# Kernel tuning notes

Hardware: AMD Instinct MI355X
Metric: run time of the kernel (lower is better)

Reference implementation:

```python
import jax, jax.numpy as jnp
import numpy as np

N = 100000          # nodes
E = 3200000         # edges per order (avg degree 32)
F_IN = 512          # num_features
HID = 128           # args.hidden
ORDER = 2
K = 10              # propagation hops
ALPHA = 0.1
C = 10              # num_classes


def setup_inputs() -> dict:
    key = jax.random.key(0)
    ks = jax.random.split(key, 10)
    x = jax.random.normal(ks[0], (N, F_IN), dtype=jnp.float32)
    edge_index1 = jax.random.randint(ks[1], (2, E), 0, N, dtype=jnp.int32)
    edge_weight1 = jax.random.uniform(ks[2], (E,), dtype=jnp.float32) / 32.0  # ~row-normalized
    edge_index2 = jax.random.randint(ks[3], (2, E), 0, N, dtype=jnp.int32)
    edge_weight2 = jax.random.uniform(ks[4], (E,), dtype=jnp.float32) / 32.0
    W_in = jax.random.normal(ks[5], (ORDER, F_IN, HID), dtype=jnp.float32) * 0.05
    b_in = jnp.zeros((ORDER, HID), dtype=jnp.float32)
    # GPR filter weights: fW[k] = alpha*(1-alpha)^k, fW[K] = (1-alpha)^K
    k_arr = np.arange(K + 1, dtype=np.float32)
    fw = ALPHA * (1.0 - ALPHA) ** k_arr
    fw[-1] = (1.0 - ALPHA) ** K
    fW = jnp.broadcast_to(jnp.asarray(fw), (ORDER, K + 1)).astype(jnp.float32)
    W_out = jax.random.normal(ks[6], (HID * ORDER, C), dtype=jnp.float32) * 0.05
    b_out = jnp.zeros((C,), dtype=jnp.float32)
    return {"x": x, "edge_index1": edge_index1, "edge_weight1": edge_weight1,
            "edge_index2": edge_index2, "edge_weight2": edge_weight2,
            "W_in": W_in, "b_in": b_in, "fW": fW, "W_out": W_out, "b_out": b_out}


def _spmm(edge_index, edge_weight, h, n):
    # y[row] += w * h[col]  (COO SpMM with add-aggregation)
    row, col = edge_index[0], edge_index[1]
    return jax.ops.segment_sum(edge_weight[:, None] * h[col], row, num_segments=n)


def reference(x, edge_index1, edge_weight1, edge_index2, edge_weight2,
              W_in, b_in, fW, W_out, b_out):
    n = x.shape[0]
    branches = [(edge_index1, edge_weight1), (edge_index2, edge_weight2)]
    outs = []
    for i, (ei, ew) in enumerate(branches):
        h = x @ W_in[i] + b_in[i]                 # [N, HID]  (dropout inactive in eval)
        hidden = h * fW[i, 0]
        for k in range(K):                        # K-hop GPR-weighted propagation
            h = _spmm(ei, ew, h, n)
            hidden = hidden + fW[i, k + 1] * h
        outs.append(hidden)
    z = jnp.concatenate(outs, axis=1) @ W_out + b_out   # [N, C]
    return jax.nn.log_softmax(z, axis=1)
```

## Files before the change

### kernel.cpp

```cpp
#include <hip/hip_runtime.h>

#define F_IN 512
#define HID 128
#define KHOPS 10
#define COUT 10
#define BM 64
#define BK 16
#define COLMASK 0x1FFFF

typedef unsigned int uint;

__device__ __forceinline__ uint f2bf1(float f) {
    uint u = __float_as_uint(f);
    return (u + 0x7fffu + ((u >> 16) & 1u)) >> 16;
}
__device__ __forceinline__ uint packbf(float a, float b) {
    return f2bf1(a) | (f2bf1(b) << 16);
}
__device__ __forceinline__ float bflo(uint u) { return __uint_as_float(u << 16); }
__device__ __forceinline__ float bfhi(uint u) { return __uint_as_float(u & 0xffff0000u); }

__global__ __launch_bounds__(256) void gemm_in_kernel(
    const float* __restrict__ x, const float* __restrict__ Win,
    const float* __restrict__ bin, uint* __restrict__ h1, uint* __restrict__ h2, int n)
{
    const int br = blockIdx.y;
    const float* W = Win + (size_t)br * F_IN * HID;
    const float* bias = bin + (size_t)br * HID;
    uint* h = br ? h2 : h1;

    __shared__ float xs[BM][BK + 1];
    __shared__ float wsb[BK][HID];
    const int t = threadIdx.x;
    const int row0 = blockIdx.x * BM;
    const int ty = t >> 4, tx = t & 15;

    float acc[4][8];
#pragma unroll
    for (int i = 0; i < 4; ++i)
#pragma unroll
        for (int j = 0; j < 8; ++j) acc[i][j] = 0.f;

    const int xr = t >> 2;
    const int xk = (t & 3) * 4;

    for (int k0 = 0; k0 < F_IN; k0 += BK) {
        float4 xv = make_float4(0.f, 0.f, 0.f, 0.f);
        if (row0 + xr < n)
            xv = *(const float4*)(x + (size_t)(row0 + xr) * F_IN + k0 + xk);
        xs[xr][xk] = xv.x; xs[xr][xk + 1] = xv.y;
        xs[xr][xk + 2] = xv.z; xs[xr][xk + 3] = xv.w;
#pragma unroll
        for (int rep = 0; rep < 2; ++rep) {
            int idx = t + rep * 256;
            int kr = idx >> 5;
            int c4 = (idx & 31) * 4;
            *(float4*)(&wsb[kr][c4]) = *(const float4*)(W + (size_t)(k0 + kr) * HID + c4);
        }
        __syncthreads();
#pragma unroll
        for (int kk = 0; kk < BK; ++kk) {
            float a0 = xs[ty * 4 + 0][kk];
            float a1 = xs[ty * 4 + 1][kk];
            float a2 = xs[ty * 4 + 2][kk];
            float a3 = xs[ty * 4 + 3][kk];
            const float4 b0 = *(const float4*)(&wsb[kk][tx * 8]);
            const float4 b1 = *(const float4*)(&wsb[kk][tx * 8 + 4]);
            acc[0][0] = fmaf(a0, b0.x, acc[0][0]); acc[0][1] = fmaf(a0, b0.y, acc[0][1]);
            acc[0][2] = fmaf(a0, b0.z, acc[0][2]); acc[0][3] = fmaf(a0, b0.w, acc[0][3]);
            acc[0][4] = fmaf(a0, b1.x, acc[0][4]); acc[0][5] = fmaf(a0, b1.y, acc[0][5]);
            acc[0][6] = fmaf(a0, b1.z, acc[0][6]); acc[0][7] = fmaf(a0, b1.w, acc[0][7]);
            acc[1][0] = fmaf(a1, b0.x, acc[1][0]); acc[1][1] = fmaf(a1, b0.y, acc[1][1]);
            acc[1][2] = fmaf(a1, b0.z, acc[1][2]); acc[1][3] = fmaf(a1, b0.w, acc[1][3]);
            acc[1][4] = fmaf(a1, b1.x, acc[1][4]); acc[1][5] = fmaf(a1, b1.y, acc[1][5]);
            acc[1][6] = fmaf(a1, b1.z, acc[1][6]); acc[1][7] = fmaf(a1, b1.w, acc[1][7]);
            acc[2][0] = fmaf(a2, b0.x, acc[2][0]); acc[2][1] = fmaf(a2, b0.y, acc[2][1]);
            acc[2][2] = fmaf(a2, b0.z, acc[2][2]); acc[2][3] = fmaf(a2, b0.w, acc[2][3]);
            acc[2][4] = fmaf(a2, b1.x, acc[2][4]); acc[2][5] = fmaf(a2, b1.y, acc[2][5]);
            acc[2][6] = fmaf(a2, b1.z, acc[2][6]); acc[2][7] = fmaf(a2, b1.w, acc[2][7]);
            acc[3][0] = fmaf(a3, b0.x, acc[3][0]); acc[3][1] = fmaf(a3, b0.y, acc[3][1]);
            acc[3][2] = fmaf(a3, b0.z, acc[3][2]); acc[3][3] = fmaf(a3, b0.w, acc[3][3]);
            acc[3][4] = fmaf(a3, b1.x, acc[3][4]); acc[3][5] = fmaf(a3, b1.y, acc[3][5]);
            acc[3][6] = fmaf(a3, b1.z, acc[3][6]); acc[3][7] = fmaf(a3, b1.w, acc[3][7]);
        }
        __syncthreads();
    }

    const float4 bv0 = *(const float4*)(bias + tx * 8);
    const float4 bv1 = *(const float4*)(bias + tx * 8 + 4);
#pragma unroll
    for (int i = 0; i < 4; ++i) {
        int row = row0 + ty * 4 + i;
        if (row >= n) continue;
        uint4 o;
        o.x = packbf(acc[i][0] + bv0.x, acc[i][1] + bv0.y);
        o.y = packbf(acc[i][2] + bv0.z, acc[i][3] + bv0.w);
        o.z = packbf(acc[i][4] + bv1.x, acc[i][5] + bv1.y);
        o.w = packbf(acc[i][6] + bv1.z, acc[i][7] + bv1.w);
        *(uint4*)(h + (size_t)row * 64 + tx * 4) = o;
    }
}


__global__ void bhist_kernel(const int* __restrict__ r1, int E1,
                             const int* __restrict__ r2, int E2,
                             int* __restrict__ bcnt, int nb)
{
    extern __shared__ int sh[];
    const int br = blockIdx.y;
    const int* rows = br ? r2 : r1;
    const int E = br ? E2 : E1;
    int* bc = bcnt + (size_t)br * nb;
    for (int i = threadIdx.x; i < nb; i += blockDim.x) sh[i] = 0;
    __syncthreads();
    for (int i = blockIdx.x * blockDim.x + threadIdx.x; i < E; i += gridDim.x * blockDim.x)
        atomicAdd(&sh[rows[i] >> 6], 1);
    __syncthreads();
    for (int i = threadIdx.x; i < nb; i += blockDim.x)
        if (sh[i]) atomicAdd(&bc[i], sh[i]);
}

__global__ __launch_bounds__(256) void bscan_kernel(
    const int* __restrict__ bcnt, int* __restrict__ bbase, int* __restrict__ bcur,
    int* __restrict__ rowp1, int* __restrict__ rowp2,
    int nb, int n, int E1, int E2)
{
    __shared__ int ssum[256];
    const int br = blockIdx.y;
    const int* bc = bcnt + (size_t)br * nb;
    int* bb = bbase + (size_t)br * (nb + 1);
    int* cur = bcur + (size_t)br * nb;
    int* rowp = br ? rowp2 : rowp1;
    const int E = br ? E2 : E1;
    const int t = threadIdx.x;
    const int chunk = (nb + 255) / 256;
    const int start = t * chunk;
    const int end = (start + chunk < nb) ? start + chunk : nb;
    int sum = 0;
    for (int i = start; i < end; ++i) sum += bc[i];
    ssum[t] = sum;
    __syncthreads();
    if (t == 0) {
        int run = 0;
        for (int i = 0; i < 256; ++i) { int v = ssum[i]; ssum[i] = run; run += v; }
        bb[nb] = E;
        rowp[n] = E;
    }
    __syncthreads();
    int run = ssum[t];
    for (int i = start; i < end; ++i) {
        bb[i] = run; cur[i] = run; run += bc[i];
    }
}

#define SCAT_BLOCKS 256
__global__ __launch_bounds__(256) void bscat_kernel(
    const int* __restrict__ r1, const int* __restrict__ c1, const float* __restrict__ w1, int E1,
    const int* __restrict__ r2, const int* __restrict__ c2, const float* __restrict__ w2, int E2,
    int* __restrict__ bcur, int2* __restrict__ t1, int2* __restrict__ t2, int nb)
{
    extern __shared__ int sh[];
    int* lh = sh;
    int* lbase = sh + nb;
    const int br = blockIdx.y;
    const int* rows = br ? r2 : r1;
    const int* cols = br ? c2 : c1;
    const float* w  = br ? w2 : w1;
    const int E = br ? E2 : E1;
    int* cur = bcur + (size_t)br * nb;
    int2* tcw = br ? t2 : t1;
    const int t = threadIdx.x;

    for (int i = t; i < nb; i += 256) lh[i] = 0;
    __syncthreads();

    const int per = (E + SCAT_BLOCKS - 1) / SCAT_BLOCKS;
    const int c0 = blockIdx.x * per;
    const int cend = (c0 + per < E) ? c0 + per : E;

    for (int i = c0 + t; i < cend; i += 256)
        atomicAdd(&lh[rows[i] >> 6], 1);
    __syncthreads();
    for (int b = t; b < nb; b += 256) {
        int c = lh[b];
        lbase[b] = c ? atomicAdd(&cur[b], c) : 0;
        lh[b] = 0;
    }
    __syncthreads();
    for (int i = c0 + t; i < cend; i += 256) {
        int r = rows[i];
        int b = r >> 6;
        int p = atomicAdd(&lh[b], 1);
        uint lo = (uint)cols[i] | ((uint)(r & 63) << 17);
        tcw[lbase[b] + p] = make_int2((int)lo, __float_as_int(w[i]));
    }
}

__global__ __launch_bounds__(256) void bsort_kernel(
    const int* __restrict__ bbase,
    const int2* __restrict__ t1, const int2* __restrict__ t2,
    int* __restrict__ rowp1, int* __restrict__ rowp2,
    int2* __restrict__ cw1, int2* __restrict__ cw2, int nb, int n)
{
    __shared__ int cnt[64], soff[64], pos[64];
    const int br = blockIdx.y;
    const int* bb = bbase + (size_t)br * (nb + 1);
    const int2* tcw = br ? t2 : t1;
    int* rowp = br ? rowp2 : rowp1;
    int2* cw = br ? cw2 : cw1;
    const int b = blockIdx.x;
    const int t = threadIdx.x;
    const int base = bb[b];
    const int m = bb[b + 1] - base;
    if (t < 64) cnt[t] = 0;
    __syncthreads();
    for (int i = t; i < m; i += 256) atomicAdd(&cnt[((uint)tcw[base + i].x >> 17) & 63], 1);
    __syncthreads();
    if (t == 0) {
        int run = 0;
#pragma unroll
        for (int r = 0; r < 64; ++r) { soff[r] = run; run += cnt[r]; }
    }
    __syncthreads();
    if (t < 64) {
        pos[t] = soff[t];
        int g = b * 64 + t;
        if (g < n) rowp[g] = base + soff[t];
    }
    __syncthreads();
    for (int i = t; i < m; i += 256) {
        int2 e = tcw[base + i];
        int r = ((uint)e.x >> 17) & 63;
        int p = atomicAdd(&pos[r], 1);
        cw[base + p] = e;
    }
}

struct BrArgs {
    const int* rowp;
    const int2* cw;
    const uint* hin;
    uint* hout;
    const float* Wo;
};

__global__ __launch_bounds__(256) void spmm2_kernel(
    BrArgs A, BrArgs B, const float* __restrict__ fW, int k,
    float* __restrict__ z2, int storeH, int n)
{
    const int bid = blockIdx.x;
    const int br = bid & 1;
    const int wid = (bid >> 1) * 4 + (threadIdx.x >> 6);
    if (wid >= n) return;
    const int*   rowp = br ? B.rowp : A.rowp;
    const int2*  cw   = br ? B.cw   : A.cw;
    const uint*  hin  = br ? B.hin  : A.hin;
    uint*        hout = br ? B.hout : A.hout;
    const float* Wo   = br ? B.Wo   : A.Wo;
    const int lane = threadIdx.x & 63;

    float w0[COUT], w1[COUT];
    const float* wp = Wo + (size_t)(lane * 2) * COUT;
#pragma unroll
    for (int c = 0; c < COUT; ++c) { w0[c] = wp[c]; w1[c] = wp[COUT + c]; }

    const int s = rowp[wid];
    const int e = rowp[wid + 1];
    const uint* hb = hin + lane;

    float2 acc = make_float2(0.f, 0.f);
    int i = s;
    while (i < e) {
        const int rem = e - i;
        const int cnt = rem < 64 ? rem : 64;
        int2 my = make_int2(0, 0);
        if (lane < cnt) my = cw[i + lane];
        int j = 0;
        for (; j + 3 < cnt; j += 4) {
            const int x0 = __builtin_amdgcn_readlane(my.x, j);
            const int y0 = __builtin_amdgcn_readlane(my.y, j);
            const int x1 = __builtin_amdgcn_readlane(my.x, j + 1);
            const int y1 = __builtin_amdgcn_readlane(my.y, j + 1);
            const int x2 = __builtin_amdgcn_readlane(my.x, j + 2);
            const int y2 = __builtin_amdgcn_readlane(my.y, j + 2);
            const int x3 = __builtin_amdgcn_readlane(my.x, j + 3);
            const int y3 = __builtin_amdgcn_readlane(my.y, j + 3);
            const uint g0 = hb[(size_t)(x0 & COLMASK) * 64];
            const uint g1 = hb[(size_t)(x1 & COLMASK) * 64];
            const uint g2 = hb[(size_t)(x2 & COLMASK) * 64];
            const uint g3 = hb[(size_t)(x3 & COLMASK) * 64];
            const float q0 = __int_as_float(y0), q1 = __int_as_float(y1);
            const float q2 = __int_as_float(y2), q3 = __int_as_float(y3);
            acc.x = fmaf(q0, bflo(g0), acc.x); acc.y = fmaf(q0, bfhi(g0), acc.y);
            acc.x = fmaf(q1, bflo(g1), acc.x); acc.y = fmaf(q1, bfhi(g1), acc.y);
            acc.x = fmaf(q2, bflo(g2), acc.x); acc.y = fmaf(q2, bfhi(g2), acc.y);
            acc.x = fmaf(q3, bflo(g3), acc.x); acc.y = fmaf(q3, bfhi(g3), acc.y);
        }
        for (; j < cnt; ++j) {
            const int xj = __builtin_amdgcn_readlane(my.x, j);
            const int yj = __builtin_amdgcn_readlane(my.y, j);
            const uint g = hb[(size_t)(xj & COLMASK) * 64];
            const float q = __int_as_float(yj);
            acc.x = fmaf(q, bflo(g), acc.x);
            acc.y = fmaf(q, bfhi(g), acc.y);
        }
        i += cnt;
    }

    if (storeH)
        hout[(size_t)wid * 64 + lane] = packbf(acc.x, acc.y);

    const float fw = fW[br * (KHOPS + 1) + k + 1];
    float zadd = 0.f;
#pragma unroll
    for (int c = 0; c < COUT; ++c) {
        float pp = fmaf(acc.x, w0[c], acc.y * w1[c]);
#pragma unroll
        for (int off = 32; off; off >>= 1) pp += __shfl_xor(pp, off);
        if (lane == c) zadd = pp;
    }
    if (lane < COUT) {
        const size_t o = (size_t)wid * (2 * COUT) + br * COUT + lane;
        z2[o] += fw * zadd;
    }
}

__global__ __launch_bounds__(256) void zacc2_kernel(
    const uint* __restrict__ h1, const uint* __restrict__ h2,
    const float* __restrict__ Wout, const float* __restrict__ fW,
    float* __restrict__ z2, int n)
{
    const int wid = (blockIdx.x * blockDim.x + threadIdx.x) >> 6;
    if (wid >= n) return;
    const int lane = threadIdx.x & 63;
    const uint u1 = h1[(size_t)wid * 64 + lane];
    const uint u2 = h2[(size_t)wid * 64 + lane];
    const float a1 = bflo(u1), b1v = bfhi(u1);
    const float a2 = bflo(u2), b2v = bfhi(u2);
    const float* wp1 = Wout + (size_t)(lane * 2) * COUT;
    const float* wp2 = Wout + (size_t)HID * COUT + (size_t)(lane * 2) * COUT;
    float zv1 = 0.f, zv2 = 0.f;
#pragma unroll
    for (int c = 0; c < COUT; ++c) {
        float p1 = fmaf(a1, wp1[c], b1v * wp1[COUT + c]);
        float p2 = fmaf(a2, wp2[c], b2v * wp2[COUT + c]);
#pragma unroll
        for (int off = 32; off; off >>= 1) { p1 += __shfl_xor(p1, off); p2 += __shfl_xor(p2, off); }
        if (lane == c) { zv1 = p1; zv2 = p2; }
    }
    if (lane < COUT) {
        z2[(size_t)wid * (2 * COUT) + lane]        = fW[0] * zv1;
        z2[(size_t)wid * (2 * COUT) + COUT + lane] = fW[KHOPS + 1] * zv2;
    }
}

__global__ void logsm_kernel(const float* __restrict__ z2, const float* __restrict__ bout,
                             float* __restrict__ out, int n)
{
    const int r = blockIdx.x * blockDim.x + threadIdx.x;
    if (r >= n) return;
    float v[COUT];
    float m = -1e30f;
#pragma unroll
    for (int c = 0; c < COUT; ++c) {
        v[c] = z2[(size_t)r * (2 * COUT) + c] + z2[(size_t)r * (2 * COUT) + COUT + c] + bout[c];
        m = fmaxf(m, v[c]);
    }
    float s = 0.f;
#pragma unroll
    for (int c = 0; c < COUT; ++c) s += expf(v[c] - m);
    const float l = logf(s) + m;
#pragma unroll
    for (int c = 0; c < COUT; ++c) out[(size_t)r * COUT + c] = v[c] - l;
}

extern "C" void kernel_launch(void* const* d_in, const int* in_sizes, int n_in,
                              void* d_out, int out_size, void* d_ws, size_t ws_size,
                              hipStream_t stream)
{
    const float* x    = (const float*)d_in[0];
    const int*   ei1  = (const int*)d_in[1];
    const float* ew1  = (const float*)d_in[2];
    const int*   ei2  = (const int*)d_in[3];
    const float* ew2  = (const float*)d_in[4];
    const float* Win  = (const float*)d_in[5];
    const float* bin  = (const float*)d_in[6];
    const float* fW   = (const float*)d_in[7];
    const float* Wout = (const float*)d_in[8];
    const float* bout = (const float*)d_in[9];
    const int n  = in_sizes[0] / F_IN;
    const int E1 = in_sizes[2];
    const int E2 = in_sizes[4];
    const int Emax = E1 > E2 ? E1 : E2;
    const int nb = (n + 63) / 64;
    float* zout = (float*)d_out;

    char* p = (char*)d_ws;
    auto alloc = [&](size_t bytes) { char* r = p; p += (bytes + 255) & ~(size_t)255; return r; };
    char* regA = alloc((size_t)4 * n * 64 * 4);
    uint* h1A = (uint*)regA;
    uint* h1B = (uint*)(regA + (size_t)n * 64 * 4);
    uint* h2A = (uint*)(regA + (size_t)2 * n * 64 * 4);
    uint* h2B = (uint*)(regA + (size_t)3 * n * 64 * 4);
    int2* tcw1 = (int2*)regA;
    int2* tcw2 = (int2*)(regA + (size_t)Emax * 8);
    int2* cw1  = (int2*)alloc((size_t)Emax * 8);
    int2* cw2  = (int2*)alloc((size_t)Emax * 8);
    int*  rowp1 = (int*)alloc((size_t)(n + 1) * 4);
    int*  rowp2 = (int*)alloc((size_t)(n + 1) * 4);
    float* z2  = (float*)alloc((size_t)n * 2 * COUT * 4);
    int*  bcnt  = (int*)alloc((size_t)2 * nb * 4);
    int*  bbase = (int*)alloc((size_t)2 * (nb + 1) * 4);
    int*  bcur  = (int*)alloc((size_t)2 * nb * 4);

    const int rowBlocks = (n + 3) / 4;

    hipMemsetAsync(bcnt, 0, (size_t)2 * nb * 4, stream);
    hipLaunchKernelGGL(bhist_kernel, dim3(256, 2), dim3(256), nb * 4, stream,
                       ei1, E1, ei2, E2, bcnt, nb);
    hipLaunchKernelGGL(bscan_kernel, dim3(1, 2), dim3(256), 0, stream,
                       bcnt, bbase, bcur, rowp1, rowp2, nb, n, E1, E2);
    hipLaunchKernelGGL(bscat_kernel, dim3(SCAT_BLOCKS, 2), dim3(256), 2 * nb * 4, stream,
                       ei1, ei1 + E1, ew1, E1, ei2, ei2 + E2, ew2, E2,
                       bcur, tcw1, tcw2, nb);
    hipLaunchKernelGGL(bsort_kernel, dim3(nb, 2), dim3(256), 0, stream,
                       bbase, tcw1, tcw2, rowp1, rowp2, cw1, cw2, nb, n);

    hipLaunchKernelGGL(gemm_in_kernel, dim3((n + BM - 1) / BM, 2), dim3(256), 0, stream,
                       x, Win, bin, h1A, h2A, n);

    hipLaunchKernelGGL(zacc2_kernel, dim3(rowBlocks), dim3(256), 0, stream,
                       h1A, h2A, Wout, fW, z2, n);

    uint* cur1 = h1A; uint* nxt1 = h1B;
    uint* cur2 = h2A; uint* nxt2 = h2B;
    for (int k = 0; k < KHOPS; ++k) {
        const int storeH = (k < KHOPS - 1) ? 1 : 0;
        BrArgs A { rowp1, cw1, cur1, nxt1, Wout };
        BrArgs B { rowp2, cw2, cur2, nxt2, Wout + (size_t)HID * COUT };
        hipLaunchKernelGGL(spmm2_kernel, dim3(rowBlocks * 2), dim3(256), 0, stream,
                           A, B, fW, k, z2, storeH, n);
        uint* t1 = cur1; cur1 = nxt1; nxt1 = t1;
        uint* t2 = cur2; cur2 = nxt2; nxt2 = t2;
    }

    hipLaunchKernelGGL(logsm_kernel, dim3((n + 255) / 256), dim3(256), 0, stream,
                       z2, bout, zout, n);
}
```

Before: 2.959 ms.

## Replace FP32 input GEMM with bf16 MFMA kernel using pre-swizzled weights

After: 2.662 ms. 10.0% less time.

```diff
diff --git a/kernel.cpp b/kernel.cpp
--- a/kernel.cpp
+++ b/kernel.cpp
@@ -4,11 +4,12 @@
 #define HID 128
 #define KHOPS 10
 #define COUT 10
-#define BM 64
-#define BK 16
 #define COLMASK 0x1FFFF
 
 typedef unsigned int uint;
+typedef unsigned short ushort;
+typedef float f32x4 __attribute__((ext_vector_type(4)));
+typedef short bf16x8 __attribute__((ext_vector_type(8)));
 
 __device__ __forceinline__ uint f2bf1(float f) {
     uint u = __float_as_uint(f);
@@ -20,87 +21,89 @@
 __device__ __forceinline__ float bflo(uint u) { return __uint_as_float(u << 16); }
 __device__ __forceinline__ float bfhi(uint u) { return __uint_as_float(u & 0xffff0000u); }
 
-__global__ __launch_bounds__(256) void gemm_in_kernel(
-    const float* __restrict__ x, const float* __restrict__ Win,
+__global__ __launch_bounds__(256) void wprep_kernel(
+    const float* __restrict__ Win, ushort* __restrict__ Wsw)
+{
+    const int t = blockIdx.x * blockDim.x + threadIdx.x;
+    if (t >= 2 * 16 * 8 * 64) return;
+    const int l = t & 63;
+    const int c = (t >> 6) & 7;
+    const int s = (t >> 9) & 15;
+    const int br = t >> 13;
+    const int col = c * 16 + (l & 15);
+    const int k0 = s * 32 + (l >> 4) * 8;
+    const float* W = Win + (size_t)br * F_IN * HID;
+    uint o0 = packbf(W[(size_t)(k0 + 0) * HID + col], W[(size_t)(k0 + 1) * HID + col]);
+    uint o1 = packbf(W[(size_t)(k0 + 2) * HID + col], W[(size_t)(k0 + 3) * HID + col]);
+    uint o2 = packbf(W[(size_t)(k0 + 4) * HID + col], W[(size_t)(k0 + 5) * HID + col]);
+    uint o3 = packbf(W[(size_t)(k0 + 6) * HID + col], W[(size_t)(k0 + 7) * HID + col]);
+    *(uint4*)(Wsw + (size_t)t * 8) = make_uint4(o0, o1, o2, o3);
+}
+
+__global__ __launch_bounds__(256) void gemm_mfma_kernel(
+    const float* __restrict__ x, const ushort* __restrict__ Wsw,
     const float* __restrict__ bin, uint* __restrict__ h1, uint* __restrict__ h2, int n)
 {
     const int br = blockIdx.y;
-    const float* W = Win + (size_t)br * F_IN * HID;
-    const float* bias = bin + (size_t)br * HID;
+    const uint4* Wb = (const uint4*)(Wsw + (size_t)br * 16 * 8 * 64 * 8);
+    const float* bias = bin + br * HID;
     uint* h = br ? h2 : h1;
 
-    __shared__ float xs[BM][BK + 1];
-    __shared__ float wsb[BK][HID];
-    const int t = threadIdx.x;
-    const int row0 = blockIdx.x * BM;
-    const int ty = t >> 4, tx = t & 15;
-
-    float acc[4][8];
-#pragma unroll
-    for (int i = 0; i < 4; ++i)
-#pragma unroll
-        for (int j = 0; j < 8; ++j) acc[i][j] = 0.f;
-
-    const int xr = t >> 2;
-    const int xk = (t & 3) * 4;
-
-    for (int k0 = 0; k0 < F_IN; k0 += BK) {
-        float4 xv = make_float4(0.f, 0.f, 0.f, 0.f);
-        if (row0 + xr < n)
-            xv = *(const float4*)(x + (size_t)(row0 + xr) * F_IN + k0 + xk);
-        xs[xr][xk] = xv.x; xs[xr][xk + 1] = xv.y;
-        xs[xr][xk + 2] = xv.z; xs[xr][xk + 3] = xv.w;
-#pragma unroll
-        for (int rep = 0; rep < 2; ++rep) {
-            int idx = t + rep * 256;
-            int kr = idx >> 5;
-            int c4 = (idx & 31) * 4;
-            *(float4*)(&wsb[kr][c4]) = *(const float4*)(W + (size_t)(k0 + kr) * HID + c4);
+    const int w = threadIdx.x >> 6;
+    const int lane = threadIdx.x & 63;
+    const int r16 = lane & 15;
+    const int kg = lane >> 4;
+
+    const int rowbase = blockIdx.x * 128 + w * 32;
+
+    f32x4 acc[2][8];
+#pragma unroll
+    for (int f = 0; f < 2; ++f)
+#pragma unroll
+        for (int c = 0; c < 8; ++c) acc[f][c] = (f32x4)0.f;
+
+    int rA0 = rowbase + r16;      if (rA0 > n - 1) rA0 = n - 1;
+    int rA1 = rowbase + 16 + r16; if (rA1 > n - 1) rA1 = n - 1;
+    const float* xp0 = x + (size_t)rA0 * F_IN + kg * 8;
+    const float* xp1 = x + (size_t)rA1 * F_IN + kg * 8;
+
+    for (int s = 0; s < 16; ++s) {
+        const float4 a0lo = *(const float4*)(xp0 + s * 32);
+        const float4 a0hi = *(const float4*)(xp0 + s * 32 + 4);
+        const float4 a1lo = *(const float4*)(xp1 + s * 32);
+        const float4 a1hi = *(const float4*)(xp1 + s * 32 + 4);
+        union { uint4 u; bf16x8 v; } af0, af1;
+        af0.u = make_uint4(packbf(a0lo.x, a0lo.y), packbf(a0lo.z, a0lo.w),
+                           packbf(a0hi.x, a0hi.y), packbf(a0hi.z, a0hi.w));
+        af1.u = make_uint4(packbf(a1lo.x, a1lo.y), packbf(a1lo.z, a1lo.w),
+                           packbf(a1hi.x, a1hi.y), packbf(a1hi.z, a1hi.w));
+        const uint4* wq = Wb + (size_t)(s * 8) * 64 + lane;
+#pragma unroll
+        for (int c = 0; c < 8; ++c) {
+            union { uint4 u; bf16x8 v; } bfr;
+            bfr.u = wq[c * 64];
+            acc[0][c] = __builtin_amdgcn_mfma_f32_16x16x32_bf16(af0.v, bfr.v, acc[0][c], 0, 0, 0);
+            acc[1][c] = __builtin_amdgcn_mfma_f32_16x16x32_bf16(af1.v, bfr.v, acc[1][c], 0, 0, 0);
         }
-        __syncthreads();
-#pragma unroll
-        for (int kk = 0; kk < BK; ++kk) {
-            float a0 = xs[ty * 4 + 0][kk];
-            float a1 = xs[ty * 4 + 1][kk];
-            float a2 = xs[ty * 4 + 2][kk];
-            float a3 = xs[ty * 4 + 3][kk];
-            const float4 b0 = *(const float4*)(&wsb[kk][tx * 8]);
-            const float4 b1 = *(const float4*)(&wsb[kk][tx * 8 + 4]);
-            acc[0][0] = fmaf(a0, b0.x, acc[0][0]); acc[0][1] = fmaf(a0, b0.y, acc[0][1]);
-            acc[0][2] = fmaf(a0, b0.z, acc[0][2]); acc[0][3] = fmaf(a0, b0.w, acc[0][3]);
-            acc[0][4] = fmaf(a0, b1.x, acc[0][4]); acc[0][5] = fmaf(a0, b1.y, acc[0][5]);
-            acc[0][6] = fmaf(a0, b1.z, acc[0][6]); acc[0][7] = fmaf(a0, b1.w, acc[0][7]);
-            acc[1][0] = fmaf(a1, b0.x, acc[1][0]); acc[1][1] = fmaf(a1, b0.y, acc[1][1]);
-            acc[1][2] = fmaf(a1, b0.z, acc[1][2]); acc[1][3] = fmaf(a1, b0.w, acc[1][3]);
-            acc[1][4] = fmaf(a1, b1.x, acc[1][4]); acc[1][5] = fmaf(a1, b1.y, acc[1][5]);
-            acc[1][6] = fmaf(a1, b1.z, acc[1][6]); acc[1][7] = fmaf(a1, b1.w, acc[1][7]);
-            acc[2][0] = fmaf(a2, b0.x, acc[2][0]); acc[2][1] = fmaf(a2, b0.y, acc[2][1]);
-            acc[2][2] = fmaf(a2, b0.z, acc[2][2]); acc[2][3] = fmaf(a2, b0.w, acc[2][3]);
-            acc[2][4] = fmaf(a2, b1.x, acc[2][4]); acc[2][5] = fmaf(a2, b1.y, acc[2][5]);
-            acc[2][6] = fmaf(a2, b1.z, acc[2][6]); acc[2][7] = fmaf(a2, b1.w, acc[2][7]);
-            acc[3][0] = fmaf(a3, b0.x, acc[3][0]); acc[3][1] = fmaf(a3, b0.y, acc[3][1]);
-            acc[3][2] = fmaf(a3, b0.z, acc[3][2]); acc[3][3] = fmaf(a3, b0.w, acc[3][3]);
-            acc[3][4] = fmaf(a3, b1.x, acc[3][4]); acc[3][5] = fmaf(a3, b1.y, acc[3][5]);
-            acc[3][6] = fmaf(a3, b1.z, acc[3][6]); acc[3][7] = fmaf(a3, b1.w, acc[3][7]);
-        }
-        __syncthreads();
-    }
-
-    const float4 bv0 = *(const float4*)(bias + tx * 8);
-    const float4 bv1 = *(const float4*)(bias + tx * 8 + 4);
-#pragma unroll
-    for (int i = 0; i < 4; ++i) {
-        int row = row0 + ty * 4 + i;
-        if (row >= n) continue;
-        uint4 o;
-        o.x = packbf(acc[i][0] + bv0.x, acc[i][1] + bv0.y);
-        o.y = packbf(acc[i][2] + bv0.z, acc[i][3] + bv0.w);
-        o.z = packbf(acc[i][4] + bv1.x, acc[i][5] + bv1.y);
-        o.w = packbf(acc[i][6] + bv1.z, acc[i][7] + bv1.w);
-        *(uint4*)(h + (size_t)row * 64 + tx * 4) = o;
-    }
-}
-
+    }
+
+    float bv[8];
+#pragma unroll
+    for (int c = 0; c < 8; ++c) bv[c] = bias[c * 16 + r16];
+
+#pragma unroll
+    for (int f = 0; f < 2; ++f)
+#pragma unroll
+        for (int c = 0; c < 8; ++c)
+#pragma unroll
+            for (int i = 0; i < 4; ++i) {
+                const float v = acc[f][c][i] + bv[c];
+                const float o = __shfl_xor(v, 1);
+                const int row = rowbase + f * 16 + kg * 4 + i;
+                if (!(lane & 1) && row < n)
+                    h[(size_t)row * 64 + c * 8 + (r16 >> 1)] = packbf(v, o);
+            }
+}
 
 __global__ void bhist_kernel(const int* __restrict__ r1, int E1,
                              const int* __restrict__ r2, int E2,
@@ -412,8 +415,11 @@
     int*  bcnt  = (int*)alloc((size_t)2 * nb * 4);
     int*  bbase = (int*)alloc((size_t)2 * (nb + 1) * 4);
     int*  bcur  = (int*)alloc((size_t)2 * nb * 4);
+    ushort* Wsw = (ushort*)alloc((size_t)2 * 16 * 8 * 64 * 8 * 2);
 
     const int rowBlocks = (n + 3) / 4;
+
+    hipLaunchKernelGGL(wprep_kernel, dim3(64), dim3(256), 0, stream, Win, Wsw);
 
     hipMemsetAsync(bcnt, 0, (size_t)2 * nb * 4, stream);
     hipLaunchKernelGGL(bhist_kernel, dim3(256, 2), dim3(256), nb * 4, stream,
@@ -426,8 +432,8 @@
     hipLaunchKernelGGL(bsort_kernel, dim3(nb, 2), dim3(256), 0, stream,
                        bbase, tcw1, tcw2, rowp1, rowp2, cw1, cw2, nb, n);
 
-    hipLaunchKernelGGL(gemm_in_kernel, dim3((n + BM - 1) / BM, 2), dim3(256), 0, stream,
-                       x, Win, bin, h1A, h2A, n);
+    hipLaunchKernelGGL(gemm_mfma_kernel, dim3((n + 127) / 128, 2), dim3(256), 0, stream,
+                       x, Wsw, bin, h1A, h2A, n);
 
     hipLaunchKernelGGL(zacc2_kernel, dim3(rowBlocks), dim3(256), 0, stream,
                        h1A, h2A, Wout, fW, z2, n);
@@ -444,6 +450,6 @@
         uint* t2 = cur2; cur2 = nxt2; nxt2 = t2;
     }
 
-    hipLaunchKernelGGL(logsm_kernel, dim3((n + 255) / 256), dim3(256), 0, stream,
+    hipLaunchKernelGGL(logsm_kernel, dim3((n + 255) / 256, 1), dim3(256), 0, stream,
                        z2, bout, zout, n);
 }
```
